# Kernel tuning notes

Hardware: AMD Instinct MI355X
Metric: run time of the kernel (lower is better)

Reference implementation:

```python
import jax, jax.numpy as jnp
import numpy as np
import math

B, H, L, D = 2, 16, 2048, 64


def setup_inputs() -> dict:
    key = jax.random.key(0)
    kq, kk, kv, km, kb = jax.random.split(key, 5)
    Q = jax.random.normal(kq, (B, H, L, D), dtype=jnp.float32)
    K = jax.random.normal(kk, (B, H, L, D), dtype=jnp.float32)
    V = jax.random.normal(kv, (B, H, L, D), dtype=jnp.float32)
    mask = jax.random.randint(km, (B, 1, L, L), 0, 2, dtype=jnp.int32)
    attn_bias = jax.random.normal(kb, (1, H, L, L), dtype=jnp.float32)
    return {"Q": Q, "K": K, "V": V, "mask": mask, "attn_bias": attn_bias,
            "last_layer_flag": 0}


def reference(Q, K, V, mask, attn_bias, last_layer_flag):
    d_tensor = K.shape[-1]
    # score: [B, H, L, L] = Q @ K^T / sqrt(d)
    score = jnp.einsum("bhqd,bhkd->bhqk", Q, K) / math.sqrt(d_tensor)
    if mask is not None:
        score = jnp.where(mask == 0, jnp.float32(-10000.0), score)
    if attn_bias is not None:
        score = score + attn_bias
    if last_layer_flag:
        return jnp.mean(score, axis=1)  # mean over heads: [B, L, L]
    score = jax.nn.softmax(score, axis=-1)
    out = jnp.einsum("bhqk,bhkd->bhqd", score, V)  # [B, H, L, D]
    return (out, score)
```

## Files before the change

### kernel.cpp

```cpp
#include <hip/hip_runtime.h>
#include <hip/hip_bf16.h>

#define Bb 2
#define Hh 16
#define Ll 2048
#define Dd 64
#define OUT_ELEMS (Bb*Hh*Ll*Dd)
#define BHL (Bb*Hh*Ll)
#define TILE 4096

typedef __attribute__((ext_vector_type(8))) short bf16x8;
typedef __attribute__((ext_vector_type(2))) short bf16x2;
typedef __attribute__((ext_vector_type(4))) float f32x4;
typedef __attribute__((ext_vector_type(2))) float f32x2;
typedef __attribute__((ext_vector_type(4))) int i32x4;
typedef __attribute__((ext_vector_type(2))) unsigned int u32x2;

__device__ __forceinline__ unsigned int pk2(float a, float b) {
    unsigned int r;
    asm("v_cvt_pk_bf16_f32 %0, %1, %2" : "=v"(r) : "v"(a), "v"(b));
    return r;
}
__device__ __forceinline__ float bf2f(short s) {
    union { float f; unsigned u; } c;
    c.u = ((unsigned)(unsigned short)s) << 16;
    return c.f;
}
__device__ __forceinline__ void bar() {
    asm volatile("s_waitcnt lgkmcnt(0)" ::: "memory");
    __builtin_amdgcn_s_barrier();
}
__device__ __forceinline__ int swz(int row, int colByte) {
    return row * 128 + (colByte ^ ((row & 7) << 4));
}

__global__ __launch_bounds__(256)
void attn_exp(const float* __restrict__ Q, const float* __restrict__ K,
              const int* __restrict__ M, const float* __restrict__ Bi,
              float* __restrict__ ws, float* __restrict__ out)
{
    __shared__ char Ks[2][64 * 128];
    __shared__ char Ps[64 * 128];

    const int bid = blockIdx.x;
    const int ks = bid & 3;
    const int b  = (bid >> 2) & 1;
    const int qt = (bid >> 3) & 31;
    const int h  = bid >> 8;
    const int q0 = qt * 64;
    const int kb = ks * 512;

    const int tid  = threadIdx.x;
    const int w    = tid >> 6;
    const int lane = tid & 63;
    const int g    = lane >> 4;
    const int c16  = lane & 15;
    const int qr   = w * 16 + c16;

    const float* Qp = Q + ((size_t)(b * Hh + h) * Ll + q0) * Dd;
    const float* Kp = K + (size_t)(b * Hh + h) * Ll * Dd;
    const int*   mrow = M  + (size_t)b * Ll * Ll + ((size_t)q0 + qr) * Ll;
    const float* brow = Bi + (size_t)h * Ll * Ll + ((size_t)q0 + qr) * Ll;
    unsigned short* Exg = (unsigned short*)(ws + 4 * (size_t)BHL);
    const size_t tb0 = (((size_t)(b * Hh + h) * 32 + qt) * 32 + (kb >> 6)) * TILE;

    if (ks == 0) {
        float* Oz = out + ((size_t)(b * Hh + h) * Ll + q0) * Dd;
        const f32x4 z = {0.f, 0.f, 0.f, 0.f};
#pragma unroll
        for (int r = 0; r < 4; ++r)
            __builtin_nontemporal_store(z, (f32x4*)(Oz + (size_t)(r * 256 + tid) * 4));
    }

    bf16x8 qf[2];
    {
        const float* qrow = Qp + qr * Dd;
#pragma unroll
        for (int kk = 0; kk < 2; ++kk) {
            f32x4 a = *(const f32x4*)(qrow + kk * 32 + g * 8);
            f32x4 c = *(const f32x4*)(qrow + kk * 32 + g * 8 + 4);
            union { bf16x8 v; unsigned int u[4]; } cvt;
            cvt.u[0] = pk2(a[0], a[1]); cvt.u[1] = pk2(a[2], a[3]);
            cvt.u[2] = pk2(c[0], c[1]); cvt.u[3] = pk2(c[2], c[3]);
            qf[kk] = cvt.v;
        }
    }

    float4 kreg[4];
    i32x4  m4[4];
    f32x4  b4[4];
    const int r0 = tid >> 4, d0 = (tid & 15) * 4;

    auto issueK = [&](int k0) {
#pragma unroll
        for (int rep = 0; rep < 4; ++rep)
            kreg[rep] = *(const float4*)(Kp + (size_t)(k0 + r0 + rep * 16) * Dd + d0);
    };
    auto writeK = [&](char* buf) {
#pragma unroll
        for (int rep = 0; rep < 4; ++rep) {
            u32x2 u = { pk2(kreg[rep].x, kreg[rep].y), pk2(kreg[rep].z, kreg[rep].w) };
            *(u32x2*)(buf + swz(r0 + rep * 16, d0 * 2)) = u;
        }
    };
    auto issueMB = [&](int k0) {
#pragma unroll
        for (int ct = 0; ct < 4; ++ct) {
            m4[ct] = *(const i32x4*)(mrow + k0 + ct * 16 + g * 4);
            b4[ct] = *(const f32x4*)(brow + k0 + ct * 16 + g * 4);
        }
    };

    issueK(kb);
    issueMB(kb);
    writeK(Ks[0]);
    issueK(kb + 64);
    bar();

    float rsv[4] = {0.f, 0.f, 0.f, 0.f};
    for (int t = 0; t < 8; ++t) {
        f32x4 sacc[4] = {{0,0,0,0},{0,0,0,0},{0,0,0,0},{0,0,0,0}};
        __builtin_amdgcn_s_setprio(1);
#pragma unroll
        for (int kk = 0; kk < 2; ++kk)
#pragma unroll
            for (int ct = 0; ct < 4; ++ct) {
                bf16x8 af = *(const bf16x8*)(Ks[t & 1] + swz(ct * 16 + c16, kk * 64 + g * 16));
                sacc[ct] = __builtin_amdgcn_mfma_f32_16x16x32_bf16(af, qf[kk], sacc[ct], 0, 0, 0);
            }
        __builtin_amdgcn_s_setprio(0);
#pragma unroll
        for (int ct = 0; ct < 4; ++ct) {
            f32x4 e;
#pragma unroll
            for (int r = 0; r < 4; ++r) {
                float s = m4[ct][r] == 0 ? -10000.0f
                                         : fmaf(sacc[ct][r], 0.125f, b4[ct][r]);
                e[r] = __expf(s);
                rsv[ct] += e[r];
            }
            u32x2 u = { pk2(e[0], e[1]), pk2(e[2], e[3]) };
            *(u32x2*)(Ps + swz(qr, ct * 32 + g * 8)) = u;
        }
        {
            unsigned short* tp = Exg + tb0 + (size_t)t * TILE + qr * 64;
#pragma unroll
            for (int half = 0; half < 2; ++half) {
                bf16x8 d = *(const bf16x8*)(Ps + swz(qr, half * 64 + g * 16));
                *(bf16x8*)(tp + half * 32 + g * 8) = d;
            }
        }
        writeK(Ks[(t + 1) & 1]);
        issueK(kb + ((t + 2) & 7) * 64);
        issueMB(kb + ((t + 1) & 7) * 64);
        bar();
    }
    float rs = (rsv[0] + rsv[1]) + (rsv[2] + rsv[3]);
    rs += __shfl_xor(rs, 16);
    rs += __shfl_xor(rs, 32);
    if (g == 0)
        ws[(size_t)ks * BHL + (size_t)(b * Hh + h) * Ll + q0 + qr] = rs;
}

__global__ __launch_bounds__(256)
void attn_pv2(const float* __restrict__ V, const float* __restrict__ ws,
              float* __restrict__ out)
{
    __shared__ char VTs[2][64 * 128];
    __shared__ char Pst[64 * 256];

    const int bid = blockIdx.x;
    const int ks = bid & 3;
    const int b  = (bid >> 2) & 1;
    const int qt = (bid >> 3) & 31;
    const int h  = bid >> 8;
    const int q0 = qt * 64;
    const int kb = ks * 512;

    const int tid  = threadIdx.x;
    const int w    = tid >> 6;
    const int lane = tid & 63;
    const int g    = lane >> 4;
    const int c16  = lane & 15;
    const int qr   = w * 16 + c16;

    const float* Vp = V + (size_t)(b * Hh + h) * Ll * Dd;
    float* Op = out + ((size_t)(b * Hh + h) * Ll + q0) * Dd;
    float* Pout = out + OUT_ELEMS + (size_t)(b * Hh + h) * Ll * Ll;
    const unsigned short* Exg = (const unsigned short*)(ws + 4 * (size_t)BHL);
    const size_t tb0 = (((size_t)(b * Hh + h) * 32 + qt) * 32 + (kb >> 6)) * TILE;

    float inv, invO[4];
    {
        size_t idx = (size_t)(b * Hh + h) * Ll + q0 + qr;
        float s = ws[idx] + ws[(size_t)BHL + idx]
                + ws[2 * (size_t)BHL + idx] + ws[3 * (size_t)BHL + idx];
        inv = 1.0f / s;
#pragma unroll
        for (int r = 0; r < 4; ++r) invO[r] = __shfl(inv, g * 4 + r);
    }

    float vreg[16];
    auto issueV = [&](int k0) {
#pragma unroll
        for (int r = 0; r < 4; ++r)
#pragma unroll
            for (int i = 0; i < 4; ++i)
                vreg[r * 4 + i] = Vp[(size_t)(k0 + w * 16 + r * 4 + i) * Dd + lane];
    };
    auto writeV = [&](char* buf) {
#pragma unroll
        for (int r = 0; r < 4; ++r) {
            u32x2 u = { pk2(vreg[r * 4 + 0], vreg[r * 4 + 1]),
                        pk2(vreg[r * 4 + 2], vreg[r * 4 + 3]) };
            *(u32x2*)(buf + swz(lane, (w * 16 + r * 4) * 2)) = u;
        }
    };

    bf16x8 pa[2];
    auto loadA = [&](int t) {
        const unsigned short* tp = Exg + tb0 + (size_t)t * TILE + qr * 64;
        pa[0] = *(const bf16x8*)(tp + g * 8);
        pa[1] = *(const bf16x8*)(tp + 32 + g * 8);
    };

    issueV(kb);
    loadA(0);
    writeV(VTs[0]);
    issueV(kb + 64);
    bar();

    f32x4 oacc[4] = {{0,0,0,0},{0,0,0,0},{0,0,0,0},{0,0,0,0}};
    for (int t = 0; t < 8; ++t) {
        __builtin_amdgcn_s_setprio(1);
#pragma unroll
        for (int kk = 0; kk < 2; ++kk)
#pragma unroll
            for (int dt = 0; dt < 4; ++dt) {
                bf16x8 vf = *(const bf16x8*)(VTs[t & 1] + swz(dt * 16 + c16, kk * 64 + g * 16));
                oacc[dt] = __builtin_amdgcn_mfma_f32_16x16x32_bf16(pa[kk], vf, oacc[dt], 0, 0, 0);
            }
        __builtin_amdgcn_s_setprio(0);
#pragma unroll
        for (int kk = 0; kk < 2; ++kk) {
            int colB = ((t & 1) * 128 + kk * 64 + g * 16) ^ ((qr & 15) << 4);
            *(bf16x8*)(Pst + qr * 256 + colB) = pa[kk];
        }
        if (t & 1) {
            const int di = t >> 1;
#pragma unroll
            for (int i = 0; i < 16; ++i) {
                const int row = w * 16 + i;
                const float rinv = __shfl(inv, i);
                const int colB = (lane * 4) ^ (i << 4);
                bf16x2 e = *(const bf16x2*)(Pst + row * 256 + colB);
                f32x2 p = { bf2f(e[0]) * rinv, bf2f(e[1]) * rinv };
                float* dst = Pout + (size_t)(q0 + row) * Ll + kb + di * 128 + lane * 2;
                __builtin_nontemporal_store(p, (f32x2*)dst);
            }
        }
        loadA((t + 1) & 7);
        writeV(VTs[(t + 1) & 1]);
        issueV(kb + ((t + 2) & 7) * 64);
        bar();
    }
#pragma unroll
    for (int dt = 0; dt < 4; ++dt)
#pragma unroll
        for (int r = 0; r < 4; ++r)
            unsafeAtomicAdd(&Op[(w * 16 + g * 4 + r) * Dd + dt * 16 + c16],
                            oacc[dt][r] * invO[r]);
}

extern "C" void kernel_launch(void* const* d_in, const int* in_sizes, int n_in,
                              void* d_out, int out_size, void* d_ws, size_t ws_size,
                              hipStream_t stream) {
    const float* Q  = (const float*)d_in[0];
    const float* K  = (const float*)d_in[1];
    const float* V  = (const float*)d_in[2];
    const int*   M  = (const int*)d_in[3];
    const float* Bi = (const float*)d_in[4];
    float* out = (float*)d_out;
    float* ws  = (float*)d_ws;

    const size_t need = 4ull * BHL * sizeof(float)
                      + (size_t)BHL * Ll * sizeof(unsigned short);
    if (ws_size >= need) {
        attn_exp<<<dim3(4096), dim3(256), 0, stream>>>(Q, K, M, Bi, ws, out);
        attn_pv2<<<dim3(4096), dim3(256), 0, stream>>>(V, ws, out);
    }
}
```

Baseline: 413.7 us.

## Recompute scores in PV pass instead of storing bf16 exp tiles to workspace

The first kernel now only computes row sums of exp(score) and no longer writes a bf16 exp matrix to workspace. The second kernel recomputes QK^T, mask and bias per tile, normalizes with the precomputed inverse sum, and feeds the result to the PV MFMA and the probability output. This removes a large workspace write and read, but the mask, bias and K are read a second time and the MFMA/exp work is duplicated.

Measured after the change: 487.4 us. 17.8% more time.

```diff
diff --git a/kernel.cpp b/kernel.cpp
--- a/kernel.cpp
+++ b/kernel.cpp
@@ -7,7 +7,6 @@
 #define Dd 64
 #define OUT_ELEMS (Bb*Hh*Ll*Dd)
 #define BHL (Bb*Hh*Ll)
-#define TILE 4096
 
 typedef __attribute__((ext_vector_type(8))) short bf16x8;
 typedef __attribute__((ext_vector_type(2))) short bf16x2;
@@ -35,12 +34,11 @@
 }
 
 __global__ __launch_bounds__(256)
-void attn_exp(const float* __restrict__ Q, const float* __restrict__ K,
-              const int* __restrict__ M, const float* __restrict__ Bi,
-              float* __restrict__ ws, float* __restrict__ out)
+void attn_rowsum(const float* __restrict__ Q, const float* __restrict__ K,
+                 const int* __restrict__ M, const float* __restrict__ Bi,
+                 float* __restrict__ ws, float* __restrict__ out)
 {
     __shared__ char Ks[2][64 * 128];
-    __shared__ char Ps[64 * 128];
 
     const int bid = blockIdx.x;
     const int ks = bid & 3;
@@ -61,8 +59,6 @@
     const float* Kp = K + (size_t)(b * Hh + h) * Ll * Dd;
     const int*   mrow = M  + (size_t)b * Ll * Ll + ((size_t)q0 + qr) * Ll;
     const float* brow = Bi + (size_t)h * Ll * Ll + ((size_t)q0 + qr) * Ll;
-    unsigned short* Exg = (unsigned short*)(ws + 4 * (size_t)BHL);
-    const size_t tb0 = (((size_t)(b * Hh + h) * 32 + qt) * 32 + (kb >> 6)) * TILE;
 
     if (ks == 0) {
         float* Oz = out + ((size_t)(b * Hh + h) * Ll + q0) * Dd;
@@ -130,26 +126,13 @@
             }
         __builtin_amdgcn_s_setprio(0);
 #pragma unroll
-        for (int ct = 0; ct < 4; ++ct) {
-            f32x4 e;
+        for (int ct = 0; ct < 4; ++ct)
 #pragma unroll
             for (int r = 0; r < 4; ++r) {
                 float s = m4[ct][r] == 0 ? -10000.0f
                                          : fmaf(sacc[ct][r], 0.125f, b4[ct][r]);
-                e[r] = __expf(s);
-                rsv[ct] += e[r];
-            }
-            u32x2 u = { pk2(e[0], e[1]), pk2(e[2], e[3]) };
-            *(u32x2*)(Ps + swz(qr, ct * 32 + g * 8)) = u;
-        }
-        {
-            unsigned short* tp = Exg + tb0 + (size_t)t * TILE + qr * 64;
-#pragma unroll
-            for (int half = 0; half < 2; ++half) {
-                bf16x8 d = *(const bf16x8*)(Ps + swz(qr, half * 64 + g * 16));
-                *(bf16x8*)(tp + half * 32 + g * 8) = d;
-            }
-        }
+                rsv[ct] += __expf(s);
+            }
         writeK(Ks[(t + 1) & 1]);
         issueK(kb + ((t + 2) & 7) * 64);
         issueMB(kb + ((t + 1) & 7) * 64);
@@ -163,9 +146,12 @@
 }
 
 __global__ __launch_bounds__(256)
-void attn_pv2(const float* __restrict__ V, const float* __restrict__ ws,
-              float* __restrict__ out)
+void attn_pv(const float* __restrict__ Q, const float* __restrict__ K,
+             const float* __restrict__ V, const int* __restrict__ M,
+             const float* __restrict__ Bi, const float* __restrict__ ws,
+             float* __restrict__ out)
 {
+    __shared__ char Ks[2][64 * 128];
     __shared__ char VTs[2][64 * 128];
     __shared__ char Pst[64 * 256];
 
@@ -184,23 +170,54 @@
     const int c16  = lane & 15;
     const int qr   = w * 16 + c16;
 
+    const float* Qp = Q + ((size_t)(b * Hh + h) * Ll + q0) * Dd;
+    const float* Kp = K + (size_t)(b * Hh + h) * Ll * Dd;
     const float* Vp = V + (size_t)(b * Hh + h) * Ll * Dd;
+    const int*   mrow = M  + (size_t)b * Ll * Ll + ((size_t)q0 + qr) * Ll;
+    const float* brow = Bi + (size_t)h * Ll * Ll + ((size_t)q0 + qr) * Ll;
     float* Op = out + ((size_t)(b * Hh + h) * Ll + q0) * Dd;
     float* Pout = out + OUT_ELEMS + (size_t)(b * Hh + h) * Ll * Ll;
-    const unsigned short* Exg = (const unsigned short*)(ws + 4 * (size_t)BHL);
-    const size_t tb0 = (((size_t)(b * Hh + h) * 32 + qt) * 32 + (kb >> 6)) * TILE;
-
-    float inv, invO[4];
+
+    float inv;
     {
         size_t idx = (size_t)(b * Hh + h) * Ll + q0 + qr;
         float s = ws[idx] + ws[(size_t)BHL + idx]
                 + ws[2 * (size_t)BHL + idx] + ws[3 * (size_t)BHL + idx];
         inv = 1.0f / s;
-#pragma unroll
-        for (int r = 0; r < 4; ++r) invO[r] = __shfl(inv, g * 4 + r);
-    }
-
-    float vreg[16];
+    }
+
+    bf16x8 qf[2];
+    {
+        const float* qrow = Qp + qr * Dd;
+#pragma unroll
+        for (int kk = 0; kk < 2; ++kk) {
+            f32x4 a = *(const f32x4*)(qrow + kk * 32 + g * 8);
+            f32x4 c = *(const f32x4*)(qrow + kk * 32 + g * 8 + 4);
+            union { bf16x8 v; unsigned int u[4]; } cvt;
+            cvt.u[0] = pk2(a[0], a[1]); cvt.u[1] = pk2(a[2], a[3]);
+            cvt.u[2] = pk2(c[0], c[1]); cvt.u[3] = pk2(c[2], c[3]);
+            qf[kk] = cvt.v;
+        }
+    }
+
+    float4 kreg[4];
+    float  vreg[16];
+    i32x4  m4[4];
+    f32x4  b4[4];
+    const int r0 = tid >> 4, d0 = (tid & 15) * 4;
+
+    auto issueK = [&](int k0) {
+#pragma unroll
+        for (int rep = 0; rep < 4; ++rep)
+            kreg[rep] = *(const float4*)(Kp + (size_t)(k0 + r0 + rep * 16) * Dd + d0);
+    };
+    auto writeK = [&](char* buf) {
+#pragma unroll
+        for (int rep = 0; rep < 4; ++rep) {
+            u32x2 u = { pk2(kreg[rep].x, kreg[rep].y), pk2(kreg[rep].z, kreg[rep].w) };
+            *(u32x2*)(buf + swz(r0 + rep * 16, d0 * 2)) = u;
+        }
+    };
     auto issueV = [&](int k0) {
 #pragma unroll
         for (int r = 0; r < 4; ++r)
@@ -216,22 +233,54 @@
             *(u32x2*)(buf + swz(lane, (w * 16 + r * 4) * 2)) = u;
         }
     };
-
-    bf16x8 pa[2];
-    auto loadA = [&](int t) {
-        const unsigned short* tp = Exg + tb0 + (size_t)t * TILE + qr * 64;
-        pa[0] = *(const bf16x8*)(tp + g * 8);
-        pa[1] = *(const bf16x8*)(tp + 32 + g * 8);
-    };
-
+    auto issueMB = [&](int k0) {
+#pragma unroll
+        for (int ct = 0; ct < 4; ++ct) {
+            m4[ct] = *(const i32x4*)(mrow + k0 + ct * 16 + g * 4);
+            b4[ct] = *(const f32x4*)(brow + k0 + ct * 16 + g * 4);
+        }
+    };
+
+    issueK(kb);
+    issueMB(kb);
     issueV(kb);
-    loadA(0);
+    writeK(Ks[0]);
     writeV(VTs[0]);
+    issueK(kb + 64);
     issueV(kb + 64);
     bar();
 
     f32x4 oacc[4] = {{0,0,0,0},{0,0,0,0},{0,0,0,0},{0,0,0,0}};
     for (int t = 0; t < 8; ++t) {
+        f32x4 sacc[4] = {{0,0,0,0},{0,0,0,0},{0,0,0,0},{0,0,0,0}};
+        __builtin_amdgcn_s_setprio(1);
+#pragma unroll
+        for (int kk = 0; kk < 2; ++kk)
+#pragma unroll
+            for (int ct = 0; ct < 4; ++ct) {
+                bf16x8 af = *(const bf16x8*)(Ks[t & 1] + swz(ct * 16 + c16, kk * 64 + g * 16));
+                sacc[ct] = __builtin_amdgcn_mfma_f32_16x16x32_bf16(af, qf[kk], sacc[ct], 0, 0, 0);
+            }
+        __builtin_amdgcn_s_setprio(0);
+#pragma unroll
+        for (int ct = 0; ct < 4; ++ct) {
+            f32x4 p;
+#pragma unroll
+            for (int r = 0; r < 4; ++r) {
+                float s = m4[ct][r] == 0 ? -10000.0f
+                                         : fmaf(sacc[ct][r], 0.125f, b4[ct][r]);
+                p[r] = __expf(s) * inv;
+            }
+            u32x2 u = { pk2(p[0], p[1]), pk2(p[2], p[3]) };
+            int colB = ((t & 1) * 128 + ct * 32 + g * 8) ^ ((qr & 15) << 4);
+            *(u32x2*)(Pst + qr * 256 + colB) = u;
+        }
+        bf16x8 pa[2];
+#pragma unroll
+        for (int kk = 0; kk < 2; ++kk) {
+            int colB = ((t & 1) * 128 + kk * 64 + g * 16) ^ ((qr & 15) << 4);
+            pa[kk] = *(const bf16x8*)(Pst + qr * 256 + colB);
+        }
         __builtin_amdgcn_s_setprio(1);
 #pragma unroll
         for (int kk = 0; kk < 2; ++kk)
@@ -241,27 +290,23 @@
                 oacc[dt] = __builtin_amdgcn_mfma_f32_16x16x32_bf16(pa[kk], vf, oacc[dt], 0, 0, 0);
             }
         __builtin_amdgcn_s_setprio(0);
-#pragma unroll
-        for (int kk = 0; kk < 2; ++kk) {
-            int colB = ((t & 1) * 128 + kk * 64 + g * 16) ^ ((qr & 15) << 4);
-            *(bf16x8*)(Pst + qr * 256 + colB) = pa[kk];
-        }
         if (t & 1) {
             const int di = t >> 1;
 #pragma unroll
             for (int i = 0; i < 16; ++i) {
                 const int row = w * 16 + i;
-                const float rinv = __shfl(inv, i);
                 const int colB = (lane * 4) ^ (i << 4);
-                bf16x2 e = *(const bf16x2*)(Pst + row * 256 + colB);
-                f32x2 p = { bf2f(e[0]) * rinv, bf2f(e[1]) * rinv };
+                bf16x2 e2 = *(const bf16x2*)(Pst + row * 256 + colB);
+                f32x2 p = { bf2f(e2[0]), bf2f(e2[1]) };
                 float* dst = Pout + (size_t)(q0 + row) * Ll + kb + di * 128 + lane * 2;
                 __builtin_nontemporal_store(p, (f32x2*)dst);
             }
         }
-        loadA((t + 1) & 7);
+        writeK(Ks[(t + 1) & 1]);
         writeV(VTs[(t + 1) & 1]);
+        issueK(kb + ((t + 2) & 7) * 64);
         issueV(kb + ((t + 2) & 7) * 64);
+        issueMB(kb + ((t + 1) & 7) * 64);
         bar();
     }
 #pragma unroll
@@ -269,7 +314,7 @@
 #pragma unroll
         for (int r = 0; r < 4; ++r)
             unsafeAtomicAdd(&Op[(w * 16 + g * 4 + r) * Dd + dt * 16 + c16],
-                            oacc[dt][r] * invO[r]);
+                            oacc[dt][r]);
 }
 
 extern "C" void kernel_launch(void* const* d_in, const int* in_sizes, int n_in,
@@ -283,10 +328,9 @@
     float* out = (float*)d_out;
     float* ws  = (float*)d_ws;
 
-    const size_t need = 4ull * BHL * sizeof(float)
-                      + (size_t)BHL * Ll * sizeof(unsigned short);
+    const size_t need = 4ull * BHL * sizeof(float);
     if (ws_size >= need) {
-        attn_exp<<<dim3(4096), dim3(256), 0, stream>>>(Q, K, M, Bi, ws, out);
-        attn_pv2<<<dim3(4096), dim3(256), 0, stream>>>(V, ws, out);
-    }
-}
+        attn_rowsum<<<dim3(4096), dim3(256), 0, stream>>>(Q, K, M, Bi, ws, out);
+        attn_pv    <<<dim3(4096), dim3(256), 0, stream>>>(Q, K, V, M, Bi, ws, out);
+    }
+}
```
